# Kernel optimization log

Hardware: AMD Instinct MI355X
Metric: run time of the kernel (lower is better)

## Reference

```python
import jax, jax.numpy as jnp
import numpy as np

N_LAYERS = 2
D_MODEL = 1024
D_INNER = 2 * D_MODEL
D_STATE = 16
D_CONV = 4
DT_RANK = D_MODEL // 16  # 64
B_SZ, L = 1, 2048
EPS = 1e-5


def layernorm(x, w, b):
    mu = jnp.mean(x, axis=-1, keepdims=True)
    var = jnp.mean(jnp.square(x - mu), axis=-1, keepdims=True)
    return (x - mu) * jax.lax.rsqrt(var + EPS) * w + b


def mamba(x, in_w, cw, cb, xp_w, dtp_w, dtp_b, A_log, Dp, out_w):
    # x: [B, L, D_MODEL]
    Bn, Ln, _ = x.shape
    xz = jnp.einsum('bld,ed->ble', x, in_w)          # [B,L,2*D_INNER]
    xc, z = jnp.split(xz, 2, axis=-1)
    # causal depthwise conv1d (kernel D_CONV)
    xp = jnp.pad(xc, ((0, 0), (D_CONV - 1, 0), (0, 0)))
    xc = sum(xp[:, k:k + Ln, :] * cw[:, k] for k in range(D_CONV)) + cb
    xc = jax.nn.silu(xc)
    dbl = jnp.einsum('ble,re->blr', xc, xp_w)        # [B,L,DT_RANK+2*D_STATE]
    dt, Bm, Cm = jnp.split(dbl, [DT_RANK, DT_RANK + D_STATE], axis=-1)
    dt = jax.nn.softplus(jnp.einsum('blr,er->ble', dt, dtp_w) + dtp_b)  # [B,L,E]
    A = -jnp.exp(A_log)                              # [E,N], strictly negative
    dA = jnp.exp(dt[..., None] * A)                  # [B,L,E,N]
    dBu = (dt * xc)[..., None] * Bm[:, :, None, :]   # [B,L,E,N]

    def step(h, inp):
        dA_t, dBu_t, C_t = inp
        h = dA_t * h + dBu_t                         # [B,E,N]
        y = jnp.einsum('ben,bn->be', h, C_t)
        return h, y

    h0 = jnp.zeros((Bn, D_INNER, D_STATE), dA.dtype)
    _, ys = jax.lax.scan(step, h0, (dA.transpose(1, 0, 2, 3),
                                    dBu.transpose(1, 0, 2, 3),
                                    Cm.transpose(1, 0, 2)))
    y = ys.transpose(1, 0, 2) + xc * Dp              # [B,L,E]
    y = y * jax.nn.silu(z)
    return jnp.einsum('ble,de->bld', y, out_w)       # [B,L,D_MODEL]


def setup_inputs() -> dict:
    key = jax.random.key(0)
    ks = jax.random.split(key, 12)
    s = 0.02
    dt_init = np.log(np.expm1(0.01)).astype(np.float32)  # softplus^-1(0.01)
    A_row = jnp.log(jnp.arange(1, D_STATE + 1, dtype=jnp.float32))
    return {
        'x': jax.random.normal(ks[0], (B_SZ, L, D_MODEL), jnp.float32),
        'ln_w': jnp.ones((N_LAYERS, D_MODEL), jnp.float32),
        'ln_b': jnp.zeros((N_LAYERS, D_MODEL), jnp.float32),
        'in_proj_w': jax.random.normal(ks[1], (N_LAYERS, 2 * D_INNER, D_MODEL)) * s,
        'conv_w': jax.random.normal(ks[2], (N_LAYERS, D_INNER, D_CONV)) * 0.2,
        'conv_b': jnp.zeros((N_LAYERS, D_INNER), jnp.float32),
        'x_proj_w': jax.random.normal(ks[3], (N_LAYERS, DT_RANK + 2 * D_STATE, D_INNER)) * s,
        'dt_proj_w': jax.random.normal(ks[4], (N_LAYERS, D_INNER, DT_RANK)) * (DT_RANK ** -0.5),
        'dt_proj_b': jnp.full((N_LAYERS, D_INNER), dt_init),
        'A_log': jnp.broadcast_to(A_row, (N_LAYERS, D_INNER, D_STATE)).copy(),
        'D_skip': jnp.ones((N_LAYERS, D_INNER), jnp.float32),
        'out_proj_w': jax.random.normal(ks[5], (N_LAYERS, D_MODEL, D_INNER)) * s,
        'norm_f_w': jnp.ones((D_MODEL,), jnp.float32),
        'norm_f_b': jnp.zeros((D_MODEL,), jnp.float32),
    }


def reference(x, ln_w, ln_b, in_proj_w, conv_w, conv_b, x_proj_w, dt_proj_w,
              dt_proj_b, A_log, D_skip, out_proj_w, norm_f_w, norm_f_b):
    for i in range(N_LAYERS):
        h = layernorm(x, ln_w[i], ln_b[i])
        h = mamba(h, in_proj_w[i], conv_w[i], conv_b[i], x_proj_w[i],
                  dt_proj_w[i], dt_proj_b[i], A_log[i], D_skip[i], out_proj_w[i])
        x = h + x  # residual (dropout/drop_path are identity in eval)
    return layernorm(x, norm_f_w, norm_f_b)
```

## Files before the change

### kernel.cpp

```cpp
#include <hip/hip_runtime.h>
#include <hip/hip_bf16.h>
#include <math.h>

#define LSEQ 2048
#define DMODEL 1024
#define DINNER 2048
#define DSTATE 16
#define DCONV 4
#define DTRANK 64
#define RPROJ 96

#define CHUNK 16
#define NCHUNK (LSEQ / CHUNK)

#define XSPLIT 4
#define XKS (DINNER / XSPLIT)

typedef __attribute__((ext_vector_type(8))) short bf16x8;
typedef __attribute__((ext_vector_type(4))) float f32x4;

__device__ __forceinline__ float softplusf(float x) {
    return (x > 20.f) ? x : log1pf(__expf(x));
}
__device__ __forceinline__ float siluf(float x) {
    return x / (1.f + __expf(-x));
}
__device__ __forceinline__ short f2bf(float f) {
    union { float f; unsigned u; } v; v.f = f;
    unsigned r = v.u + 0x7FFFu + ((v.u >> 16) & 1u);
    return (short)(r >> 16);
}
__device__ __forceinline__ float bf2f(short h) {
    union { unsigned u; float f; } v;
    v.u = ((unsigned)(unsigned short)h) << 16;
    return v.f;
}

__device__ __forceinline__ void cvt8(const float* __restrict__ s,
                                     short* __restrict__ d, int i) {
    const float4 a = *(const float4*)(s + i);
    const float4 b = *(const float4*)(s + i + 4);
    alignas(16) short h[8];
    h[0] = f2bf(a.x); h[1] = f2bf(a.y); h[2] = f2bf(a.z); h[3] = f2bf(a.w);
    h[4] = f2bf(b.x); h[5] = f2bf(b.y); h[6] = f2bf(b.z); h[7] = f2bf(b.w);
    *(uint4*)(d + i) = *(const uint4*)h;
}

__device__ __forceinline__ void ln_phase(
    const float* __restrict__ x, const float* __restrict__ w,
    const float* __restrict__ b, float* __restrict__ outf,
    short* __restrict__ outb, int bid, int tid)
{
    const int wv = tid >> 6, lane = tid & 63;
    const int row = bid * 4 + wv;
    const float* xr = x + (size_t)row * DMODEL;
    float v[16];
    float s = 0.f, sq = 0.f;
#pragma unroll
    for (int k = 0; k < 16; k++) {
        v[k] = xr[k * 64 + lane];
        s += v[k];
        sq += v[k] * v[k];
    }
#pragma unroll
    for (int off = 32; off > 0; off >>= 1) {
        s += __shfl_xor(s, off, 64);
        sq += __shfl_xor(sq, off, 64);
    }
    const float mu = s * (1.f / DMODEL);
    const float var = sq * (1.f / DMODEL) - mu * mu;
    const float rstd = rsqrtf(var + 1e-5f);
#pragma unroll
    for (int k = 0; k < 16; k++) {
        const int i = k * 64 + lane;
        const float o = (v[k] - mu) * rstd * w[i] + b[i];
        if (outf) outf[(size_t)row * DMODEL + i] = o;
        else      outb[(size_t)row * DMODEL + i] = f2bf(o);
    }
}

__global__ __launch_bounds__(256) void cvt_ln_kernel(
    const float* __restrict__ in_w, short* __restrict__ in_w_bf,
    const float* __restrict__ xp_w, short* __restrict__ xp_w_bf,
    const float* __restrict__ out_w, short* __restrict__ out_w_bf,
    const float* __restrict__ dtp_w, short* __restrict__ dtp_w_bf,
    const float* __restrict__ x_in, const float* __restrict__ ln_w,
    const float* __restrict__ ln_b, short* __restrict__ h_bf)
{
    const int n1 = 2 * (2 * DINNER) * DMODEL;
    const int n2 = 2 * RPROJ * DINNER;
    const int n3 = 2 * DMODEL * DINNER;
    const int bid = blockIdx.x;
    const int tid = threadIdx.x;
    {
        int i = (bid * 256 + tid) * 8;
        if (i < n1) { cvt8(in_w, in_w_bf, i); goto done_cvt; }
        i -= n1;
        if (i < n2) { cvt8(xp_w, xp_w_bf, i); goto done_cvt; }
        i -= n2;
        if (i < n3) { cvt8(out_w, out_w_bf, i); goto done_cvt; }
        i -= n3;
        cvt8(dtp_w, dtp_w_bf, i);
    }
done_cvt:
    if (bid < LSEQ / 4)
        ln_phase(x_in, ln_w, ln_b, nullptr, h_bf, bid, tid);
}

__global__ __launch_bounds__(256) void ln_g(
    const float* __restrict__ x, const float* __restrict__ w,
    const float* __restrict__ b, float* __restrict__ outf,
    short* __restrict__ outb)
{
    ln_phase(x, w, b, outf, outb, blockIdx.x, threadIdx.x);
}

template<int MI, int NJ, int MODE>
__global__ __launch_bounds__(256) void gemm_g(
    const short* __restrict__ A, int lda,
    const short* __restrict__ W, int ldw,
    float* __restrict__ Cf, short* __restrict__ Cb, int ldc,
    int N, int K, const float* __restrict__ resid,
    float* __restrict__ zbuf, int zcount4)
{
    constexpr int BM = 32 * MI;
    constexpr int BN = 32 * NJ;
    constexpr int AISS = BM / 32;
    constexpr int WISS = BN / 32;
    __shared__ alignas(16) short As[BM * 64];
    __shared__ alignas(16) short Ws[BN * 64];

    const int tid = threadIdx.x;
    const int lane = tid & 63;
    const int w = tid >> 6;
    const int wr = w >> 1, wc = w & 1;
    const int row0 = blockIdx.y * BM;
    const int col0 = blockIdx.x * BN;

    const int srow = tid >> 3;
    const int dch  = tid & 7;
    const int skch = (dch ^ (srow & 7)) * 8;

    f32x4 acc[MI][NJ];
#pragma unroll
    for (int i = 0; i < MI; i++)
#pragma unroll
        for (int j = 0; j < NJ; j++) acc[i][j] = (f32x4)0.f;

    const int lrow = lane & 15;
    const int q = lane >> 4;

    for (int kt = 0; kt < K; kt += 64) {
        __syncthreads();
#pragma unroll
        for (int j = 0; j < AISS; j++) {
            const short* gp = A + (size_t)(row0 + j * 32 + srow) * lda + kt + skch;
            __builtin_amdgcn_global_load_lds(
                (const __attribute__((address_space(1))) void*)gp,
                (__attribute__((address_space(3))) void*)(&As[j * 2048 + tid * 8]),
                16, 0, 0);
        }
#pragma unroll
        for (int j = 0; j < WISS; j++) {
            const int wrow = col0 + j * 32 + srow;
            if (wrow < N) {
                const short* gp = W + (size_t)wrow * ldw + kt + skch;
                __builtin_amdgcn_global_load_lds(
                    (const __attribute__((address_space(1))) void*)gp,
                    (__attribute__((address_space(3))) void*)(&Ws[j * 2048 + tid * 8]),
                    16, 0, 0);
            }
        }
        __syncthreads();

#pragma unroll
        for (int ks = 0; ks < 2; ks++) {
            bf16x8 af[MI], bfr[NJ];
#pragma unroll
            for (int i = 0; i < MI; i++) {
                const int R = wr * (16 * MI) + i * 16 + lrow;
                const int pc = (ks * 4 + q) ^ (R & 7);
                af[i] = *(const bf16x8*)&As[R * 64 + pc * 8];
            }
#pragma unroll
            for (int j = 0; j < NJ; j++) {
                const int R = wc * (16 * NJ) + j * 16 + lrow;
                const int pc = (ks * 4 + q) ^ (R & 7);
                bfr[j] = *(const bf16x8*)&Ws[R * 64 + pc * 8];
            }
#pragma unroll
            for (int i = 0; i < MI; i++)
#pragma unroll
                for (int j = 0; j < NJ; j++)
                    acc[i][j] = __builtin_amdgcn_mfma_f32_16x16x32_bf16(
                        af[i], bfr[j], acc[i][j], 0, 0, 0);
        }
    }

    const int rbase = row0 + wr * (16 * MI);
    const int cbase = col0 + wc * (16 * NJ);
#pragma unroll
    for (int i = 0; i < MI; i++) {
#pragma unroll
        for (int j = 0; j < NJ; j++) {
            const int gcol = cbase + j * 16 + lrow;
            if (gcol < N) {
#pragma unroll
                for (int r = 0; r < 4; r++) {
                    const int grow = rbase + i * 16 + (lane >> 4) * 4 + r;
                    float v = acc[i][j][r];
                    if (MODE == 2) {
                        Cf[(size_t)grow * ldc + gcol] =
                            v + resid[(size_t)grow * ldc + gcol];
                    } else {
                        Cb[(size_t)grow * ldc + gcol] = f2bf(v);
                    }
                }
            }
        }
    }
    if (zbuf) {
        const int g = (blockIdx.y * gridDim.x + blockIdx.x) * 256 + tid;
        if (g < zcount4)
            *(float4*)(zbuf + (size_t)g * 4) = make_float4(0.f, 0.f, 0.f, 0.f);
    }
}

__global__ __launch_bounds__(256) void xproj_conv_g(
    const short* __restrict__ xzb,
    const float* __restrict__ cw,
    const float* __restrict__ cb,
    const short* __restrict__ W,
    float* __restrict__ dbl)
{
    __shared__ alignas(16) short As[64 * 64];
    __shared__ alignas(16) short Ws[64 * 64];
    __shared__ float cw4[XKS][4];
    __shared__ float cbl[XKS];

    const int tid = threadIdx.x;
    const int lane = tid & 63;
    const int w = tid >> 6;
    const int wr = w >> 1, wc = w & 1;
    const int row0 = blockIdx.y * 64;
    const int col0 = blockIdx.x * 64;
    const int kbeg = blockIdx.z * XKS;
    const int srow = tid >> 3;
    const int dch  = tid & 7;
    const int skch = (dch ^ (srow & 7)) * 8;
    const int lrow = lane & 15;
    const int q = lane >> 4;

    {
        const float4* cwsrc = (const float4*)cw;
        *(float4*)&cw4[tid * 2][0]     = cwsrc[kbeg + tid * 2];
        *(float4*)&cw4[tid * 2 + 1][0] = cwsrc[kbeg + tid * 2 + 1];
        cbl[tid]       = cb[kbeg + tid];
        cbl[tid + 256] = cb[kbeg + tid + 256];
    }

    f32x4 acc[2][2];
#pragma unroll
    for (int i = 0; i < 2; i++)
#pragma unroll
        for (int j = 0; j < 2; j++) acc[i][j] = (f32x4)0.f;

    for (int kt = kbeg; kt < kbeg + XKS; kt += 64) {
        __syncthreads();
#pragma unroll
        for (int j = 0; j < 2; j++) {
            const int t = row0 + j * 32 + srow;
            const int ch0 = kt + skch;
            const int lc = ch0 - kbeg;
            float a8[8];
#pragma unroll
            for (int i = 0; i < 8; i++) a8[i] = cbl[lc + i];
#pragma unroll
            for (int k = 0; k < DCONV; k++) {
                const int tt = t - (DCONV - 1) + k;
                if (tt >= 0) {
                    const bf16x8 v = *(const bf16x8*)(xzb + (size_t)tt * (2 * DINNER) + ch0);
#pragma unroll
                    for (int i = 0; i < 8; i++)
                        a8[i] += bf2f(v[i]) * cw4[lc + i][k];
                }
            }
            alignas(16) short h8[8];
#pragma unroll
            for (int i = 0; i < 8; i++) h8[i] = f2bf(siluf(a8[i]));
            *(uint4*)(&As[j * 2048 + tid * 8]) = *(const uint4*)h8;
        }
#pragma unroll
        for (int j = 0; j < 2; j++) {
            const int wrow = col0 + j * 32 + srow;
            if (wrow < RPROJ) {
                const short* gp = W + (size_t)wrow * DINNER + kt + skch;
                __builtin_amdgcn_global_load_lds(
                    (const __attribute__((address_space(1))) void*)gp,
                    (__attribute__((address_space(3))) void*)(&Ws[j * 2048 + tid * 8]),
                    16, 0, 0);
            }
        }
        __syncthreads();

#pragma unroll
        for (int ks = 0; ks < 2; ks++) {
            bf16x8 af[2], bfr[2];
#pragma unroll
            for (int i = 0; i < 2; i++) {
                const int R = wr * 32 + i * 16 + lrow;
                const int pc = (ks * 4 + q) ^ (R & 7);
                af[i] = *(const bf16x8*)&As[R * 64 + pc * 8];
            }
#pragma unroll
            for (int j = 0; j < 2; j++) {
                const int R = wc * 32 + j * 16 + lrow;
                const int pc = (ks * 4 + q) ^ (R & 7);
                bfr[j] = *(const bf16x8*)&Ws[R * 64 + pc * 8];
            }
#pragma unroll
            for (int i = 0; i < 2; i++)
#pragma unroll
                for (int j = 0; j < 2; j++)
                    acc[i][j] = __builtin_amdgcn_mfma_f32_16x16x32_bf16(
                        af[i], bfr[j], acc[i][j], 0, 0, 0);
        }
    }

    const int rbase = row0 + wr * 32;
    const int cbase = col0 + wc * 32;
#pragma unroll
    for (int i = 0; i < 2; i++)
#pragma unroll
        for (int j = 0; j < 2; j++) {
            const int gcol = cbase + j * 16 + lrow;
            if (gcol < RPROJ) {
#pragma unroll
                for (int r = 0; r < 4; r++) {
                    const int grow = rbase + i * 16 + (lane >> 4) * 4 + r;
                    atomicAdd(&dbl[(size_t)grow * RPROJ + gcol], acc[i][j][r]);
                }
            }
        }
}

__global__ __launch_bounds__(256) void dtproj_g(
    const float* __restrict__ dbl,
    const short* __restrict__ dtp_w,
    const float* __restrict__ dtp_b,
    short* __restrict__ dt_bf)
{
    __shared__ alignas(16) short As[64 * 32];
    __shared__ alignas(16) short Ws[128 * 32];
    const int tid = threadIdx.x;
    const int lane = tid & 63;
    const int w = tid >> 6;
    const int wr = w >> 1, wc = w & 1;
    const int row0 = blockIdx.y * 64;
    const int col0 = blockIdx.x * 128;
    const int srow = tid >> 2;
    const int skch = ((tid & 3) ^ ((srow >> 1) & 3)) * 8;
    const int lrow = lane & 15;
    const int q = lane >> 4;

    f32x4 acc[2][4];
#pragma unroll
    for (int i = 0; i < 2; i++)
#pragma unroll
        for (int j = 0; j < 4; j++) acc[i][j] = (f32x4)0.f;

#pragma unroll
    for (int kt = 0; kt < 64; kt += 32) {
        __syncthreads();
        {
            const float* gp = dbl + (size_t)(row0 + srow) * RPROJ + kt + skch;
            const float4 a = *(const float4*)gp;
            const float4 b = *(const float4*)(gp + 4);
            alignas(16) short h[8];
            h[0] = f2bf(a.x); h[1] = f2bf(a.y); h[2] = f2bf(a.z); h[3] = f2bf(a.w);
            h[4] = f2bf(b.x); h[5] = f2bf(b.y); h[6] = f2bf(b.z); h[7] = f2bf(b.w);
            *(uint4*)(As + tid * 8) = *(const uint4*)h;
        }
#pragma unroll
        for (int j = 0; j < 2; j++) {
            const short* gp = dtp_w + (size_t)(col0 + j * 64 + srow) * DTRANK + kt + skch;
            __builtin_amdgcn_global_load_lds(
                (const __attribute__((address_space(1))) void*)gp,
                (__attribute__((address_space(3))) void*)(&Ws[j * 2048 + tid * 8]),
                16, 0, 0);
        }
        __syncthreads();

        bf16x8 af[2], bfr[4];
#pragma unroll
        for (int i = 0; i < 2; i++) {
            const int R = wr * 32 + i * 16 + lrow;
            af[i] = *(const bf16x8*)&As[R * 32 + ((q ^ ((R >> 1) & 3)) * 8)];
        }
#pragma unroll
        for (int j = 0; j < 4; j++) {
            const int R = wc * 64 + j * 16 + lrow;
            bfr[j] = *(const bf16x8*)&Ws[R * 32 + ((q ^ ((R >> 1) & 3)) * 8)];
        }
#pragma unroll
        for (int i = 0; i < 2; i++)
#pragma unroll
            for (int j = 0; j < 4; j++)
                acc[i][j] = __builtin_amdgcn_mfma_f32_16x16x32_bf16(
                    af[i], bfr[j], acc[i][j], 0, 0, 0);
    }

    const int rbase = row0 + wr * 32;
    const int cbase = col0 + wc * 64;
#pragma unroll
    for (int i = 0; i < 2; i++)
#pragma unroll
        for (int j = 0; j < 4; j++) {
            const int gcol = cbase + j * 16 + lrow;
#pragma unroll
            for (int r = 0; r < 4; r++) {
                const int grow = rbase + i * 16 + (lane >> 4) * 4 + r;
                dt_bf[(size_t)grow * DINNER + gcol] =
                    f2bf(softplusf(acc[i][j][r] + dtp_b[gcol]));
            }
        }
}

__global__ __launch_bounds__(256) void scan1_g(
    const short* __restrict__ dtb,
    const short* __restrict__ xzb,
    const float* __restrict__ cw,
    const float* __restrict__ cb,
    const float* __restrict__ dbl,
    const float* __restrict__ A_log,
    float* __restrict__ S,
    float* __restrict__ sumdt)
{
    const int e = blockIdx.x * 256 + threadIdx.x;
    const int c = blockIdx.y;
    float a[DSTATE];
#pragma unroll
    for (int n = 0; n < DSTATE; n++) a[n] = -__expf(A_log[(size_t)e * DSTATE + n]);
    float h[DSTATE];
#pragma unroll
    for (int n = 0; n < DSTATE; n++) h[n] = 0.f;
    float sd = 0.f;

    __shared__ float sBC[CHUNK][32];
    for (int i = threadIdx.x; i < CHUNK * 32; i += 256) {
        const int tl = i >> 5, j = i & 31;
        sBC[tl][j] = dbl[(size_t)(c * CHUNK + tl) * RPROJ + DTRANK + j];
    }
    __syncthreads();

    const float4 cwv = *(const float4*)(cw + (size_t)e * 4);
    const float cbv = cb[e];
    const size_t rb = (size_t)c * CHUNK * DINNER + e;
    const size_t xzr = (size_t)c * CHUNK * (2 * DINNER) + e;
    float w1 = 0.f, w2 = 0.f, w3 = 0.f;
    if (c > 0) {
        w1 = bf2f(xzb[xzr - 1 * (2 * DINNER)]);
        w2 = bf2f(xzb[xzr - 2 * (2 * DINNER)]);
        w3 = bf2f(xzb[xzr - 3 * (2 * DINNER)]);
    }
    float w0 = bf2f(xzb[xzr]);
    short dt_c = dtb[rb];
#pragma unroll
    for (int tl = 0; tl < CHUNK; tl++) {
        short dt_n = 0; float xz_n = 0.f;
        if (tl + 1 < CHUNK) {
            dt_n = dtb[rb + (size_t)(tl + 1) * DINNER];
            xz_n = bf2f(xzb[xzr + (size_t)(tl + 1) * (2 * DINNER)]);
        }
        const float xcv = siluf(cbv + cwv.x * w3 + cwv.y * w2 + cwv.z * w1 + cwv.w * w0);
        const float dtv = bf2f(dt_c);
        const float du = dtv * xcv;
        sd += dtv;
#pragma unroll
        for (int n = 0; n < DSTATE; n++) {
            const float dA = __expf(dtv * a[n]);
            h[n] = dA * h[n] + du * sBC[tl][n];
        }
        w3 = w2; w2 = w1; w1 = w0; w0 = xz_n; dt_c = dt_n;
    }
    sumdt[(size_t)c * DINNER + e] = sd;
#pragma unroll
    for (int n = 0; n < DSTATE; n++)
        S[((size_t)c * DSTATE + n) * DINNER + e] = h[n];
}

__global__ __launch_bounds__(256) void scan2_g(
    const float* __restrict__ A_log,
    const float* __restrict__ sumdt,
    float* __restrict__ S)
{
    const int idx = blockIdx.x * 256 + threadIdx.x;
    const int e = idx & (DINNER - 1);
    const int n = idx >> 11;
    const float a = -__expf(A_log[(size_t)e * DSTATE + n]);
    const size_t base = (size_t)n * DINNER + e;
    const size_t cstr = (size_t)DSTATE * DINNER;
    float H = 0.f;
    for (int c = 0; c < NCHUNK; c += 4) {
        const float sc0 = S[base + (size_t)(c + 0) * cstr];
        const float sc1 = S[base + (size_t)(c + 1) * cstr];
        const float sc2 = S[base + (size_t)(c + 2) * cstr];
        const float sc3 = S[base + (size_t)(c + 3) * cstr];
        const float sd0 = sumdt[(size_t)(c + 0) * DINNER + e];
        const float sd1 = sumdt[(size_t)(c + 1) * DINNER + e];
        const float sd2 = sumdt[(size_t)(c + 2) * DINNER + e];
        const float sd3 = sumdt[(size_t)(c + 3) * DINNER + e];
        S[base + (size_t)(c + 0) * cstr] = H;
        H = __expf(a * sd0) * H + sc0;
        S[base + (size_t)(c + 1) * cstr] = H;
        H = __expf(a * sd1) * H + sc1;
        S[base + (size_t)(c + 2) * cstr] = H;
        H = __expf(a * sd2) * H + sc2;
        S[base + (size_t)(c + 3) * cstr] = H;
        H = __expf(a * sd3) * H + sc3;
    }
}

__global__ __launch_bounds__(256) void scan3_g(
    const short* __restrict__ dtb,
    const short* __restrict__ xzb,
    const float* __restrict__ cw,
    const float* __restrict__ cb,
    const float* __restrict__ dbl,
    const float* __restrict__ A_log,
    const float* __restrict__ Dp,
    const float* __restrict__ S,
    short* __restrict__ yb)
{
    const int e = blockIdx.x * 256 + threadIdx.x;
    const int c = blockIdx.y;
    float a[DSTATE];
#pragma unroll
    for (int n = 0; n < DSTATE; n++) a[n] = -__expf(A_log[(size_t)e * DSTATE + n]);
    float h[DSTATE];
#pragma unroll
    for (int n = 0; n < DSTATE; n++)
        h[n] = S[((size_t)c * DSTATE + n) * DINNER + e];
    const float dskip = Dp[e];

    __shared__ float sBC[CHUNK][32];
    for (int i = threadIdx.x; i < CHUNK * 32; i += 256) {
        const int tl = i >> 5, j = i & 31;
        sBC[tl][j] = dbl[(size_t)(c * CHUNK + tl) * RPROJ + DTRANK + j];
    }
    __syncthreads();

    const float4 cwv = *(const float4*)(cw + (size_t)e * 4);
    const float cbv = cb[e];
    const size_t rb = (size_t)c * CHUNK * DINNER + e;
    const size_t xzr = (size_t)c * CHUNK * (2 * DINNER) + e;
    const size_t zb = xzr + DINNER;
    float w1 = 0.f, w2 = 0.f, w3 = 0.f;
    if (c > 0) {
        w1 = bf2f(xzb[xzr - 1 * (2 * DINNER)]);
        w2 = bf2f(xzb[xzr - 2 * (2 * DINNER)]);
        w3 = bf2f(xzb[xzr - 3 * (2 * DINNER)]);
    }
    float w0 = bf2f(xzb[xzr]);
    short dt_c = dtb[rb], z_c = xzb[zb];
#pragma unroll
    for (int tl = 0; tl < CHUNK; tl++) {
        short dt_n = 0, z_n = 0; float xz_n = 0.f;
        if (tl + 1 < CHUNK) {
            dt_n = dtb[rb + (size_t)(tl + 1) * DINNER];
            xz_n = bf2f(xzb[xzr + (size_t)(tl + 1) * (2 * DINNER)]);
            z_n = xzb[zb + (size_t)(tl + 1) * (2 * DINNER)];
        }
        const float xcv = siluf(cbv + cwv.x * w3 + cwv.y * w2 + cwv.z * w1 + cwv.w * w0);
        const float dtv = bf2f(dt_c);
        const float du = dtv * xcv;
        float yv = 0.f;
#pragma unroll
        for (int n = 0; n < DSTATE; n++) {
            const float dA = __expf(dtv * a[n]);
            h[n] = dA * h[n] + du * sBC[tl][n];
            yv += h[n] * sBC[tl][16 + n];
        }
        yv = (yv + xcv * dskip) * siluf(bf2f(z_c));
        yb[rb + (size_t)tl * DINNER] = f2bf(yv);
        w3 = w2; w2 = w1; w1 = w0; w0 = xz_n; dt_c = dt_n; z_c = z_n;
    }
}

extern "C" void kernel_launch(void* const* d_in, const int* in_sizes, int n_in,
                              void* d_out, int out_size, void* d_ws, size_t ws_size,
                              hipStream_t stream) {
    const float* x_in   = (const float*)d_in[0];
    const float* ln_w   = (const float*)d_in[1];
    const float* ln_b   = (const float*)d_in[2];
    const float* in_w   = (const float*)d_in[3];
    const float* conv_w = (const float*)d_in[4];
    const float* conv_b = (const float*)d_in[5];
    const float* xp_w   = (const float*)d_in[6];
    const float* dtp_w  = (const float*)d_in[7];
    const float* dtp_b  = (const float*)d_in[8];
    const float* A_log  = (const float*)d_in[9];
    const float* D_skip = (const float*)d_in[10];
    const float* out_w  = (const float*)d_in[11];
    const float* nf_w   = (const float*)d_in[12];
    const float* nf_b   = (const float*)d_in[13];
    float* out = (float*)d_out;

    float* w = (float*)d_ws;
    float* buf_x = w; w += (size_t)LSEQ * DMODEL;
    float* dbl   = w; w += (size_t)LSEQ * RPROJ;
    float* Sbuf  = w; w += (size_t)NCHUNK * DSTATE * DINNER;
    float* sumdt = w; w += (size_t)NCHUNK * DINNER;
    short* h_bf    = (short*)w; w += (size_t)LSEQ * DMODEL / 2;
    short* xz_bf   = (short*)w; w += (size_t)LSEQ * 2 * DINNER / 2;
    short* dt_bf   = (short*)w; w += (size_t)LSEQ * DINNER / 2;
    short* y_bf    = (short*)w; w += (size_t)LSEQ * DINNER / 2;
    short* in_w_bf  = (short*)w; w += (size_t)2 * (2 * DINNER) * DMODEL / 2;
    short* xp_w_bf  = (short*)w; w += (size_t)2 * RPROJ * DINNER / 2;
    short* dtp_w_bf = (short*)w; w += (size_t)2 * DINNER * DTRANK / 2;
    short* out_w_bf = (short*)w; w += (size_t)2 * DMODEL * DINNER / 2;

    {
        const int total = 2 * (2 * DINNER) * DMODEL + 2 * RPROJ * DINNER
                        + 2 * DMODEL * DINNER + 2 * DINNER * DTRANK;
        cvt_ln_kernel<<<dim3(total / (256 * 8)), dim3(256), 0, stream>>>(
            in_w, in_w_bf, xp_w, xp_w_bf, out_w, out_w_bf, dtp_w, dtp_w_bf,
            x_in, ln_w, ln_b, h_bf);
    }

    for (int layer = 0; layer < 2; layer++) {
        const float* resid_src = (layer == 0) ? x_in : buf_x;
        const float* cwl = conv_w + (size_t)layer * DINNER * DCONV;
        const float* cbl = conv_b + (size_t)layer * DINNER;
        if (layer > 0)
            ln_g<<<dim3(LSEQ / 4), dim3(256), 0, stream>>>(
                resid_src, ln_w + layer * DMODEL, ln_b + layer * DMODEL,
                nullptr, h_bf);
        gemm_g<4, 4, 3><<<dim3((2 * DINNER) / 128, LSEQ / 128), dim3(256), 0, stream>>>(
            h_bf, DMODEL, in_w_bf + (size_t)layer * 2 * DINNER * DMODEL, DMODEL,
            nullptr, xz_bf, 2 * DINNER, 2 * DINNER, DMODEL, nullptr,
            dbl, (LSEQ * RPROJ) / 4);
        xproj_conv_g<<<dim3(2, LSEQ / 64, XSPLIT), dim3(256), 0, stream>>>(
            xz_bf, cwl, cbl, xp_w_bf + (size_t)layer * RPROJ * DINNER, dbl);
        dtproj_g<<<dim3(DINNER / 128, LSEQ / 64), dim3(256), 0, stream>>>(
            dbl, dtp_w_bf + (size_t)layer * DINNER * DTRANK,
            dtp_b + layer * DINNER, dt_bf);
        const float* Al = A_log + (size_t)layer * DINNER * DSTATE;
        scan1_g<<<dim3(DINNER / 256, NCHUNK), dim3(256), 0, stream>>>(
            dt_bf, xz_bf, cwl, cbl, dbl, Al, Sbuf, sumdt);
        scan2_g<<<dim3((DINNER * DSTATE) / 256), dim3(256), 0, stream>>>(
            Al, sumdt, Sbuf);
        scan3_g<<<dim3(DINNER / 256, NCHUNK), dim3(256), 0, stream>>>(
            dt_bf, xz_bf, cwl, cbl, dbl, Al, D_skip + layer * DINNER, Sbuf, y_bf);
        gemm_g<4, 2, 2><<<dim3(DMODEL / 64, LSEQ / 128), dim3(256), 0, stream>>>(
            y_bf, DINNER, out_w_bf + (size_t)layer * DMODEL * DINNER, DINNER,
            buf_x, nullptr, DMODEL, DMODEL, DINNER, resid_src,
            nullptr, 0);
    }
    ln_g<<<dim3(LSEQ / 4), dim3(256), 0, stream>>>(buf_x, nf_w, nf_b, out, nullptr);
}
```

Measured before the change: 457.8 us.

## Fuse dt projection GEMM into scan kernels and drop dt buffer

Removes the separate dtproj kernel and instead computes the dt projection (MFMA over the 64-wide dt rank plus softplus) inside both scan1 and scan3 for each chunk, storing dt in LDS. This eliminates one kernel launch per layer and the global write and reads of the bf16 dt buffer. In exchange, the small dt GEMM is computed twice (once per scan pass), the dt_proj weights are read straight from global memory without LDS staging, and each scan kernel needs extra LDS and a barrier.

```diff
diff --git a/kernel.cpp b/kernel.cpp
--- a/kernel.cpp
+++ b/kernel.cpp
@@ -344,90 +344,9 @@
         }
 }
 
-__global__ __launch_bounds__(256) void dtproj_g(
-    const float* __restrict__ dbl,
+__global__ __launch_bounds__(256) void scan1_g(
     const short* __restrict__ dtp_w,
     const float* __restrict__ dtp_b,
-    short* __restrict__ dt_bf)
-{
-    __shared__ alignas(16) short As[64 * 32];
-    __shared__ alignas(16) short Ws[128 * 32];
-    const int tid = threadIdx.x;
-    const int lane = tid & 63;
-    const int w = tid >> 6;
-    const int wr = w >> 1, wc = w & 1;
-    const int row0 = blockIdx.y * 64;
-    const int col0 = blockIdx.x * 128;
-    const int srow = tid >> 2;
-    const int skch = ((tid & 3) ^ ((srow >> 1) & 3)) * 8;
-    const int lrow = lane & 15;
-    const int q = lane >> 4;
-
-    f32x4 acc[2][4];
-#pragma unroll
-    for (int i = 0; i < 2; i++)
-#pragma unroll
-        for (int j = 0; j < 4; j++) acc[i][j] = (f32x4)0.f;
-
-#pragma unroll
-    for (int kt = 0; kt < 64; kt += 32) {
-        __syncthreads();
-        {
-            const float* gp = dbl + (size_t)(row0 + srow) * RPROJ + kt + skch;
-            const float4 a = *(const float4*)gp;
-            const float4 b = *(const float4*)(gp + 4);
-            alignas(16) short h[8];
-            h[0] = f2bf(a.x); h[1] = f2bf(a.y); h[2] = f2bf(a.z); h[3] = f2bf(a.w);
-            h[4] = f2bf(b.x); h[5] = f2bf(b.y); h[6] = f2bf(b.z); h[7] = f2bf(b.w);
-            *(uint4*)(As + tid * 8) = *(const uint4*)h;
-        }
-#pragma unroll
-        for (int j = 0; j < 2; j++) {
-            const short* gp = dtp_w + (size_t)(col0 + j * 64 + srow) * DTRANK + kt + skch;
-            __builtin_amdgcn_global_load_lds(
-                (const __attribute__((address_space(1))) void*)gp,
-                (__attribute__((address_space(3))) void*)(&Ws[j * 2048 + tid * 8]),
-                16, 0, 0);
-        }
-        __syncthreads();
-
-        bf16x8 af[2], bfr[4];
-#pragma unroll
-        for (int i = 0; i < 2; i++) {
-            const int R = wr * 32 + i * 16 + lrow;
-            af[i] = *(const bf16x8*)&As[R * 32 + ((q ^ ((R >> 1) & 3)) * 8)];
-        }
-#pragma unroll
-        for (int j = 0; j < 4; j++) {
-            const int R = wc * 64 + j * 16 + lrow;
-            bfr[j] = *(const bf16x8*)&Ws[R * 32 + ((q ^ ((R >> 1) & 3)) * 8)];
-        }
-#pragma unroll
-        for (int i = 0; i < 2; i++)
-#pragma unroll
-            for (int j = 0; j < 4; j++)
-                acc[i][j] = __builtin_amdgcn_mfma_f32_16x16x32_bf16(
-                    af[i], bfr[j], acc[i][j], 0, 0, 0);
-    }
-
-    const int rbase = row0 + wr * 32;
-    const int cbase = col0 + wc * 64;
-#pragma unroll
-    for (int i = 0; i < 2; i++)
-#pragma unroll
-        for (int j = 0; j < 4; j++) {
-            const int gcol = cbase + j * 16 + lrow;
-#pragma unroll
-            for (int r = 0; r < 4; r++) {
-                const int grow = rbase + i * 16 + (lane >> 4) * 4 + r;
-                dt_bf[(size_t)grow * DINNER + gcol] =
-                    f2bf(softplusf(acc[i][j][r] + dtp_b[gcol]));
-            }
-        }
-}
-
-__global__ __launch_bounds__(256) void scan1_g(
-    const short* __restrict__ dtb,
     const short* __restrict__ xzb,
     const float* __restrict__ cw,
     const float* __restrict__ cb,
@@ -436,8 +355,65 @@
     float* __restrict__ S,
     float* __restrict__ sumdt)
 {
-    const int e = blockIdx.x * 256 + threadIdx.x;
+    __shared__ alignas(16) short Ad[CHUNK * 64];
+    __shared__ short dt_lds[CHUNK * 256];
+    __shared__ float sBC[CHUNK][32];
+
+    const int tid = threadIdx.x;
+    const int eb = blockIdx.x;
     const int c = blockIdx.y;
+    const int e = eb * 256 + tid;
+    const int lane = tid & 63;
+    const int wv = tid >> 6;
+    const int lrow = lane & 15;
+    const int q = lane >> 4;
+
+    if (tid < CHUNK * 8) {
+        const int row = tid >> 3, dch = tid & 7;
+        const float* gp = dbl + (size_t)(c * CHUNK + row) * RPROJ
+                        + ((dch ^ (row & 7)) * 8);
+        const float4 a = *(const float4*)gp;
+        const float4 b = *(const float4*)(gp + 4);
+        alignas(16) short h8[8];
+        h8[0] = f2bf(a.x); h8[1] = f2bf(a.y); h8[2] = f2bf(a.z); h8[3] = f2bf(a.w);
+        h8[4] = f2bf(b.x); h8[5] = f2bf(b.y); h8[6] = f2bf(b.z); h8[7] = f2bf(b.w);
+        *(uint4*)(&Ad[row * 64 + dch * 8]) = *(const uint4*)h8;
+    }
+    for (int i = tid; i < CHUNK * 32; i += 256) {
+        const int tl = i >> 5, j = i & 31;
+        sBC[tl][j] = dbl[(size_t)(c * CHUNK + tl) * RPROJ + DTRANK + j];
+    }
+    __syncthreads();
+
+    {
+        f32x4 dacc[4];
+#pragma unroll
+        for (int j = 0; j < 4; j++) dacc[j] = (f32x4)0.f;
+#pragma unroll
+        for (int ks = 0; ks < 2; ks++) {
+            const int pcA = ((ks * 4 + q) ^ (lrow & 7)) * 8;
+            const bf16x8 af = *(const bf16x8*)&Ad[lrow * 64 + pcA];
+#pragma unroll
+            for (int j = 0; j < 4; j++) {
+                const int ej = eb * 256 + wv * 64 + j * 16 + lrow;
+                const bf16x8 bw = *(const bf16x8*)(
+                    dtp_w + (size_t)ej * DTRANK + (ks * 4 + q) * 8);
+                dacc[j] = __builtin_amdgcn_mfma_f32_16x16x32_bf16(
+                    af, bw, dacc[j], 0, 0, 0);
+            }
+        }
+#pragma unroll
+        for (int j = 0; j < 4; j++) {
+            const int ecol = wv * 64 + j * 16 + lrow;
+            const float bias = dtp_b[eb * 256 + ecol];
+#pragma unroll
+            for (int r = 0; r < 4; r++)
+                dt_lds[(q * 4 + r) * 256 + ecol] =
+                    f2bf(softplusf(dacc[j][r] + bias));
+        }
+    }
+    __syncthreads();
+
     float a[DSTATE];
 #pragma unroll
     for (int n = 0; n < DSTATE; n++) a[n] = -__expf(A_log[(size_t)e * DSTATE + n]);
@@ -446,16 +422,8 @@
     for (int n = 0; n < DSTATE; n++) h[n] = 0.f;
     float sd = 0.f;
 
-    __shared__ float sBC[CHUNK][32];
-    for (int i = threadIdx.x; i < CHUNK * 32; i += 256) {
-        const int tl = i >> 5, j = i & 31;
-        sBC[tl][j] = dbl[(size_t)(c * CHUNK + tl) * RPROJ + DTRANK + j];
-    }
-    __syncthreads();
-
     const float4 cwv = *(const float4*)(cw + (size_t)e * 4);
     const float cbv = cb[e];
-    const size_t rb = (size_t)c * CHUNK * DINNER + e;
     const size_t xzr = (size_t)c * CHUNK * (2 * DINNER) + e;
     float w1 = 0.f, w2 = 0.f, w3 = 0.f;
     if (c > 0) {
@@ -464,16 +432,13 @@
         w3 = bf2f(xzb[xzr - 3 * (2 * DINNER)]);
     }
     float w0 = bf2f(xzb[xzr]);
-    short dt_c = dtb[rb];
 #pragma unroll
     for (int tl = 0; tl < CHUNK; tl++) {
-        short dt_n = 0; float xz_n = 0.f;
-        if (tl + 1 < CHUNK) {
-            dt_n = dtb[rb + (size_t)(tl + 1) * DINNER];
+        float xz_n = 0.f;
+        if (tl + 1 < CHUNK)
             xz_n = bf2f(xzb[xzr + (size_t)(tl + 1) * (2 * DINNER)]);
-        }
         const float xcv = siluf(cbv + cwv.x * w3 + cwv.y * w2 + cwv.z * w1 + cwv.w * w0);
-        const float dtv = bf2f(dt_c);
+        const float dtv = bf2f(dt_lds[tl * 256 + tid]);
         const float du = dtv * xcv;
         sd += dtv;
 #pragma unroll
@@ -481,7 +446,7 @@
             const float dA = __expf(dtv * a[n]);
             h[n] = dA * h[n] + du * sBC[tl][n];
         }
-        w3 = w2; w2 = w1; w1 = w0; w0 = xz_n; dt_c = dt_n;
+        w3 = w2; w2 = w1; w1 = w0; w0 = xz_n;
     }
     sumdt[(size_t)c * DINNER + e] = sd;
 #pragma unroll
@@ -522,7 +487,8 @@
 }
 
 __global__ __launch_bounds__(256) void scan3_g(
-    const short* __restrict__ dtb,
+    const short* __restrict__ dtp_w,
+    const float* __restrict__ dtp_b,
     const short* __restrict__ xzb,
     const float* __restrict__ cw,
     const float* __restrict__ cb,
@@ -532,8 +498,65 @@
     const float* __restrict__ S,
     short* __restrict__ yb)
 {
-    const int e = blockIdx.x * 256 + threadIdx.x;
+    __shared__ alignas(16) short Ad[CHUNK * 64];
+    __shared__ short dt_lds[CHUNK * 256];
+    __shared__ float sBC[CHUNK][32];
+
+    const int tid = threadIdx.x;
+    const int eb = blockIdx.x;
     const int c = blockIdx.y;
+    const int e = eb * 256 + tid;
+    const int lane = tid & 63;
+    const int wv = tid >> 6;
+    const int lrow = lane & 15;
+    const int q = lane >> 4;
+
+    if (tid < CHUNK * 8) {
+        const int row = tid >> 3, dch = tid & 7;
+        const float* gp = dbl + (size_t)(c * CHUNK + row) * RPROJ
+                        + ((dch ^ (row & 7)) * 8);
+        const float4 a = *(const float4*)gp;
+        const float4 b = *(const float4*)(gp + 4);
+        alignas(16) short h8[8];
+        h8[0] = f2bf(a.x); h8[1] = f2bf(a.y); h8[2] = f2bf(a.z); h8[3] = f2bf(a.w);
+        h8[4] = f2bf(b.x); h8[5] = f2bf(b.y); h8[6] = f2bf(b.z); h8[7] = f2bf(b.w);
+        *(uint4*)(&Ad[row * 64 + dch * 8]) = *(const uint4*)h8;
+    }
+    for (int i = tid; i < CHUNK * 32; i += 256) {
+        const int tl = i >> 5, j = i & 31;
+        sBC[tl][j] = dbl[(size_t)(c * CHUNK + tl) * RPROJ + DTRANK + j];
+    }
+    __syncthreads();
+
+    {
+        f32x4 dacc[4];
+#pragma unroll
+        for (int j = 0; j < 4; j++) dacc[j] = (f32x4)0.f;
+#pragma unroll
+        for (int ks = 0; ks < 2; ks++) {
+            const int pcA = ((ks * 4 + q) ^ (lrow & 7)) * 8;
+            const bf16x8 af = *(const bf16x8*)&Ad[lrow * 64 + pcA];
+#pragma unroll
+            for (int j = 0; j < 4; j++) {
+                const int ej = eb * 256 + wv * 64 + j * 16 + lrow;
+                const bf16x8 bw = *(const bf16x8*)(
+                    dtp_w + (size_t)ej * DTRANK + (ks * 4 + q) * 8);
+                dacc[j] = __builtin_amdgcn_mfma_f32_16x16x32_bf16(
+                    af, bw, dacc[j], 0, 0, 0);
+            }
+        }
+#pragma unroll
+        for (int j = 0; j < 4; j++) {
+            const int ecol = wv * 64 + j * 16 + lrow;
+            const float bias = dtp_b[eb * 256 + ecol];
+#pragma unroll
+            for (int r = 0; r < 4; r++)
+                dt_lds[(q * 4 + r) * 256 + ecol] =
+                    f2bf(softplusf(dacc[j][r] + bias));
+        }
+    }
+    __syncthreads();
+
     float a[DSTATE];
 #pragma unroll
     for (int n = 0; n < DSTATE; n++) a[n] = -__expf(A_log[(size_t)e * DSTATE + n]);
@@ -542,13 +565,6 @@
     for (int n = 0; n < DSTATE; n++)
         h[n] = S[((size_t)c * DSTATE + n) * DINNER + e];
     const float dskip = Dp[e];
-
-    __shared__ float sBC[CHUNK][32];
-    for (int i = threadIdx.x; i < CHUNK * 32; i += 256) {
-        const int tl = i >> 5, j = i & 31;
-        sBC[tl][j] = dbl[(size_t)(c * CHUNK + tl) * RPROJ + DTRANK + j];
-    }
-    __syncthreads();
 
     const float4 cwv = *(const float4*)(cw + (size_t)e * 4);
     const float cbv = cb[e];
@@ -562,17 +578,16 @@
         w3 = bf2f(xzb[xzr - 3 * (2 * DINNER)]);
     }
     float w0 = bf2f(xzb[xzr]);
-    short dt_c = dtb[rb], z_c = xzb[zb];
+    short z_c = xzb[zb];
 #pragma unroll
     for (int tl = 0; tl < CHUNK; tl++) {
-        short dt_n = 0, z_n = 0; float xz_n = 0.f;
+        short z_n = 0; float xz_n = 0.f;
         if (tl + 1 < CHUNK) {
-            dt_n = dtb[rb + (size_t)(tl + 1) * DINNER];
             xz_n = bf2f(xzb[xzr + (size_t)(tl + 1) * (2 * DINNER)]);
             z_n = xzb[zb + (size_t)(tl + 1) * (2 * DINNER)];
         }
         const float xcv = siluf(cbv + cwv.x * w3 + cwv.y * w2 + cwv.z * w1 + cwv.w * w0);
-        const float dtv = bf2f(dt_c);
+        const float dtv = bf2f(dt_lds[tl * 256 + tid]);
         const float du = dtv * xcv;
         float yv = 0.f;
 #pragma unroll
@@ -583,7 +598,7 @@
         }
         yv = (yv + xcv * dskip) * siluf(bf2f(z_c));
         yb[rb + (size_t)tl * DINNER] = f2bf(yv);
-        w3 = w2; w2 = w1; w1 = w0; w0 = xz_n; dt_c = dt_n; z_c = z_n;
+        w3 = w2; w2 = w1; w1 = w0; w0 = xz_n; z_c = z_n;
     }
 }
 
@@ -613,7 +628,6 @@
     float* sumdt = w; w += (size_t)NCHUNK * DINNER;
     short* h_bf    = (short*)w; w += (size_t)LSEQ * DMODEL / 2;
     short* xz_bf   = (short*)w; w += (size_t)LSEQ * 2 * DINNER / 2;
-    short* dt_bf   = (short*)w; w += (size_t)LSEQ * DINNER / 2;
     short* y_bf    = (short*)w; w += (size_t)LSEQ * DINNER / 2;
     short* in_w_bf  = (short*)w; w += (size_t)2 * (2 * DINNER) * DMODEL / 2;
     short* xp_w_bf  = (short*)w; w += (size_t)2 * RPROJ * DINNER / 2;
@@ -632,6 +646,8 @@
         const float* resid_src = (layer == 0) ? x_in : buf_x;
         const float* cwl = conv_w + (size_t)layer * DINNER * DCONV;
         const float* cbl = conv_b + (size_t)layer * DINNER;
+        const short* dtwl = dtp_w_bf + (size_t)layer * DINNER * DTRANK;
+        const float* dtbl = dtp_b + (size_t)layer * DINNER;
         if (layer > 0)
             ln_g<<<dim3(LSEQ / 4), dim3(256), 0, stream>>>(
                 resid_src, ln_w + layer * DMODEL, ln_b + layer * DMODEL,
@@ -642,16 +658,14 @@
             dbl, (LSEQ * RPROJ) / 4);
         xproj_conv_g<<<dim3(2, LSEQ / 64, XSPLIT), dim3(256), 0, stream>>>(
             xz_bf, cwl, cbl, xp_w_bf + (size_t)layer * RPROJ * DINNER, dbl);
-        dtproj_g<<<dim3(DINNER / 128, LSEQ / 64), dim3(256), 0, stream>>>(
-            dbl, dtp_w_bf + (size_t)layer * DINNER * DTRANK,
-            dtp_b + layer * DINNER, dt_bf);
         const float* Al = A_log + (size_t)layer * DINNER * DSTATE;
         scan1_g<<<dim3(DINNER / 256, NCHUNK), dim3(256), 0, stream>>>(
-            dt_bf, xz_bf, cwl, cbl, dbl, Al, Sbuf, sumdt);
+            dtwl, dtbl, xz_bf, cwl, cbl, dbl, Al, Sbuf, sumdt);
         scan2_g<<<dim3((DINNER * DSTATE) / 256), dim3(256), 0, stream>>>(
             Al, sumdt, Sbuf);
         scan3_g<<<dim3(DINNER / 256, NCHUNK), dim3(256), 0, stream>>>(
-            dt_bf, xz_bf, cwl, cbl, dbl, Al, D_skip + layer * DINNER, Sbuf, y_bf);
+            dtwl, dtbl, xz_bf, cwl, cbl, dbl, Al, D_skip + layer * DINNER,
+            Sbuf, y_bf);
         gemm_g<4, 2, 2><<<dim3(DMODEL / 64, LSEQ / 128), dim3(256), 0, stream>>>(
             y_bf, DINNER, out_w_bf + (size_t)layer * DMODEL * DINNER, DINNER,
             buf_x, nullptr, DMODEL, DMODEL, DINNER, resid_src,
```

After: 507.7 us. 1.11x slower.

## Parallelize chunked scan over state dimension with one thread per (channel,state)

Applied to the files above, without the earlier changes.

Scan1 and scan3 now use one thread per (channel, state) pair instead of one thread per channel looping over 16 states. Each block covers 16 channels and stages dt, the conv+silu output and silu(z) in shared memory. The y reduction over states uses wave shuffles, and the transposes for S and y go through shared memory. The aim is 16x more threads and less register pressure from the serial per-thread state loop, at the cost of 16x more blocks, redundant staging loads and shuffle reductions.

```diff
diff --git a/kernel.cpp b/kernel.cpp
--- a/kernel.cpp
+++ b/kernel.cpp
@@ -436,57 +436,57 @@
     float* __restrict__ S,
     float* __restrict__ sumdt)
 {
-    const int e = blockIdx.x * 256 + threadIdx.x;
+    __shared__ float dt_s[CHUNK][16];
+    __shared__ float xc_s[CHUNK][16];
+    __shared__ float sBC[CHUNK][32];
+    __shared__ float hT[16 * 17];
+
+    const int tid = threadIdx.x;
+    const int e0 = blockIdx.x * 16;
     const int c = blockIdx.y;
-    float a[DSTATE];
-#pragma unroll
-    for (int n = 0; n < DSTATE; n++) a[n] = -__expf(A_log[(size_t)e * DSTATE + n]);
-    float h[DSTATE];
-#pragma unroll
-    for (int n = 0; n < DSTATE; n++) h[n] = 0.f;
-    float sd = 0.f;
-
-    __shared__ float sBC[CHUNK][32];
-    for (int i = threadIdx.x; i < CHUNK * 32; i += 256) {
+
+    {
+        const int t = tid >> 4, el = tid & 15;
+        const int tg = c * CHUNK + t;
+        const int e = e0 + el;
+        dt_s[t][el] = bf2f(dtb[(size_t)tg * DINNER + e]);
+        const float4 cwv = *(const float4*)(cw + (size_t)e * 4);
+        const float cwk[4] = { cwv.x, cwv.y, cwv.z, cwv.w };
+        float acc = cb[e];
+#pragma unroll
+        for (int k = 0; k < DCONV; k++) {
+            const int tt = tg - (DCONV - 1) + k;
+            if (tt >= 0)
+                acc += bf2f(xzb[(size_t)tt * (2 * DINNER) + e]) * cwk[k];
+        }
+        xc_s[t][el] = siluf(acc);
+    }
+    for (int i = tid; i < CHUNK * 32; i += 256) {
         const int tl = i >> 5, j = i & 31;
         sBC[tl][j] = dbl[(size_t)(c * CHUNK + tl) * RPROJ + DTRANK + j];
     }
     __syncthreads();
 
-    const float4 cwv = *(const float4*)(cw + (size_t)e * 4);
-    const float cbv = cb[e];
-    const size_t rb = (size_t)c * CHUNK * DINNER + e;
-    const size_t xzr = (size_t)c * CHUNK * (2 * DINNER) + e;
-    float w1 = 0.f, w2 = 0.f, w3 = 0.f;
-    if (c > 0) {
-        w1 = bf2f(xzb[xzr - 1 * (2 * DINNER)]);
-        w2 = bf2f(xzb[xzr - 2 * (2 * DINNER)]);
-        w3 = bf2f(xzb[xzr - 3 * (2 * DINNER)]);
-    }
-    float w0 = bf2f(xzb[xzr]);
-    short dt_c = dtb[rb];
+    const int el2 = tid >> 4;
+    const int n = tid & 15;
+    const int e2 = e0 + el2;
+    const float a = -__expf(A_log[(size_t)e2 * DSTATE + n]);
+    float h = 0.f, sd = 0.f;
 #pragma unroll
     for (int tl = 0; tl < CHUNK; tl++) {
-        short dt_n = 0; float xz_n = 0.f;
-        if (tl + 1 < CHUNK) {
-            dt_n = dtb[rb + (size_t)(tl + 1) * DINNER];
-            xz_n = bf2f(xzb[xzr + (size_t)(tl + 1) * (2 * DINNER)]);
-        }
-        const float xcv = siluf(cbv + cwv.x * w3 + cwv.y * w2 + cwv.z * w1 + cwv.w * w0);
-        const float dtv = bf2f(dt_c);
-        const float du = dtv * xcv;
+        const float dtv = dt_s[tl][el2];
+        const float du = dtv * xc_s[tl][el2];
         sd += dtv;
-#pragma unroll
-        for (int n = 0; n < DSTATE; n++) {
-            const float dA = __expf(dtv * a[n]);
-            h[n] = dA * h[n] + du * sBC[tl][n];
-        }
-        w3 = w2; w2 = w1; w1 = w0; w0 = xz_n; dt_c = dt_n;
-    }
-    sumdt[(size_t)c * DINNER + e] = sd;
-#pragma unroll
-    for (int n = 0; n < DSTATE; n++)
-        S[((size_t)c * DSTATE + n) * DINNER + e] = h[n];
+        const float dA = __expf(dtv * a);
+        h = dA * h + du * sBC[tl][n];
+    }
+    if (n == 0) sumdt[(size_t)c * DINNER + e2] = sd;
+    hT[el2 * 17 + n] = h;
+    __syncthreads();
+    {
+        const int n2 = tid >> 4, e3 = tid & 15;
+        S[((size_t)c * DSTATE + n2) * DINNER + e0 + e3] = hT[e3 * 17 + n2];
+    }
 }
 
 __global__ __launch_bounds__(256) void scan2_g(
@@ -532,58 +532,69 @@
     const float* __restrict__ S,
     short* __restrict__ yb)
 {
-    const int e = blockIdx.x * 256 + threadIdx.x;
+    __shared__ float dt_s[CHUNK][16];
+    __shared__ float xc_s[CHUNK][16];
+    __shared__ float sz_s[CHUNK][16];
+    __shared__ float sBC[CHUNK][32];
+    __shared__ float hT[16 * 17];
+    __shared__ short y_s[CHUNK][16];
+
+    const int tid = threadIdx.x;
+    const int e0 = blockIdx.x * 16;
     const int c = blockIdx.y;
-    float a[DSTATE];
-#pragma unroll
-    for (int n = 0; n < DSTATE; n++) a[n] = -__expf(A_log[(size_t)e * DSTATE + n]);
-    float h[DSTATE];
-#pragma unroll
-    for (int n = 0; n < DSTATE; n++)
-        h[n] = S[((size_t)c * DSTATE + n) * DINNER + e];
-    const float dskip = Dp[e];
-
-    __shared__ float sBC[CHUNK][32];
-    for (int i = threadIdx.x; i < CHUNK * 32; i += 256) {
+
+    {
+        const int t = tid >> 4, el = tid & 15;
+        const int tg = c * CHUNK + t;
+        const int e = e0 + el;
+        dt_s[t][el] = bf2f(dtb[(size_t)tg * DINNER + e]);
+        sz_s[t][el] = siluf(bf2f(xzb[(size_t)tg * (2 * DINNER) + DINNER + e]));
+        const float4 cwv = *(const float4*)(cw + (size_t)e * 4);
+        const float cwk[4] = { cwv.x, cwv.y, cwv.z, cwv.w };
+        float acc = cb[e];
+#pragma unroll
+        for (int k = 0; k < DCONV; k++) {
+            const int tt = tg - (DCONV - 1) + k;
+            if (tt >= 0)
+                acc += bf2f(xzb[(size_t)tt * (2 * DINNER) + e]) * cwk[k];
+        }
+        xc_s[t][el] = siluf(acc);
+    }
+    for (int i = tid; i < CHUNK * 32; i += 256) {
         const int tl = i >> 5, j = i & 31;
         sBC[tl][j] = dbl[(size_t)(c * CHUNK + tl) * RPROJ + DTRANK + j];
     }
+    {
+        const int n2 = tid >> 4, e3 = tid & 15;
+        hT[e3 * 17 + n2] = S[((size_t)c * DSTATE + n2) * DINNER + e0 + e3];
+    }
     __syncthreads();
 
-    const float4 cwv = *(const float4*)(cw + (size_t)e * 4);
-    const float cbv = cb[e];
-    const size_t rb = (size_t)c * CHUNK * DINNER + e;
-    const size_t xzr = (size_t)c * CHUNK * (2 * DINNER) + e;
-    const size_t zb = xzr + DINNER;
-    float w1 = 0.f, w2 = 0.f, w3 = 0.f;
-    if (c > 0) {
-        w1 = bf2f(xzb[xzr - 1 * (2 * DINNER)]);
-        w2 = bf2f(xzb[xzr - 2 * (2 * DINNER)]);
-        w3 = bf2f(xzb[xzr - 3 * (2 * DINNER)]);
-    }
-    float w0 = bf2f(xzb[xzr]);
-    short dt_c = dtb[rb], z_c = xzb[zb];
+    const int el2 = tid >> 4;
+    const int n = tid & 15;
+    const int e2 = e0 + el2;
+    const float a = -__expf(A_log[(size_t)e2 * DSTATE + n]);
+    float h = hT[el2 * 17 + n];
+    const float dskip = Dp[e2];
 #pragma unroll
     for (int tl = 0; tl < CHUNK; tl++) {
-        short dt_n = 0, z_n = 0; float xz_n = 0.f;
-        if (tl + 1 < CHUNK) {
-            dt_n = dtb[rb + (size_t)(tl + 1) * DINNER];
-            xz_n = bf2f(xzb[xzr + (size_t)(tl + 1) * (2 * DINNER)]);
-            z_n = xzb[zb + (size_t)(tl + 1) * (2 * DINNER)];
-        }
-        const float xcv = siluf(cbv + cwv.x * w3 + cwv.y * w2 + cwv.z * w1 + cwv.w * w0);
-        const float dtv = bf2f(dt_c);
+        const float dtv = dt_s[tl][el2];
+        const float xcv = xc_s[tl][el2];
         const float du = dtv * xcv;
-        float yv = 0.f;
-#pragma unroll
-        for (int n = 0; n < DSTATE; n++) {
-            const float dA = __expf(dtv * a[n]);
-            h[n] = dA * h[n] + du * sBC[tl][n];
-            yv += h[n] * sBC[tl][16 + n];
-        }
-        yv = (yv + xcv * dskip) * siluf(bf2f(z_c));
-        yb[rb + (size_t)tl * DINNER] = f2bf(yv);
-        w3 = w2; w2 = w1; w1 = w0; w0 = xz_n; dt_c = dt_n; z_c = z_n;
+        const float dA = __expf(dtv * a);
+        h = dA * h + du * sBC[tl][n];
+        float yp = h * sBC[tl][16 + n];
+        yp += __shfl_xor(yp, 8, 64);
+        yp += __shfl_xor(yp, 4, 64);
+        yp += __shfl_xor(yp, 2, 64);
+        yp += __shfl_xor(yp, 1, 64);
+        if (n == 0)
+            y_s[tl][el2] = f2bf((yp + xcv * dskip) * sz_s[tl][el2]);
+    }
+    __syncthreads();
+    {
+        const int t = tid >> 4, el = tid & 15;
+        yb[((size_t)(c * CHUNK + t)) * DINNER + e0 + el] = y_s[t][el];
     }
 }
 
@@ -646,12 +657,13 @@
             dbl, dtp_w_bf + (size_t)layer * DINNER * DTRANK,
             dtp_b + layer * DINNER, dt_bf);
         const float* Al = A_log + (size_t)layer * DINNER * DSTATE;
-        scan1_g<<<dim3(DINNER / 256, NCHUNK), dim3(256), 0, stream>>>(
+        scan1_g<<<dim3(DINNER / 16, NCHUNK), dim3(256), 0, stream>>>(
             dt_bf, xz_bf, cwl, cbl, dbl, Al, Sbuf, sumdt);
         scan2_g<<<dim3((DINNER * DSTATE) / 256), dim3(256), 0, stream>>>(
             Al, sumdt, Sbuf);
-        scan3_g<<<dim3(DINNER / 256, NCHUNK), dim3(256), 0, stream>>>(
-            dt_bf, xz_bf, cwl, cbl, dbl, Al, D_skip + layer * DINNER, Sbuf, y_bf);
+        scan3_g<<<dim3(DINNER / 16, NCHUNK), dim3(256), 0, stream>>>(
+            dt_bf, xz_bf, cwl, cbl, dbl, Al, D_skip + layer * DINNER,
+            Sbuf, y_bf);
         gemm_g<4, 2, 2><<<dim3(DMODEL / 64, LSEQ / 128), dim3(256), 0, stream>>>(
             y_bf, DINNER, out_w_bf + (size_t)layer * DMODEL * DINNER, DINNER,
             buf_x, nullptr, DMODEL, DMODEL, DINNER, resid_src,
```

Measured after the change: 594.6 us. +29.9%, slower.
